# Kernel optimization log

Hardware: AMD Instinct MI355X
Metric: run time of the kernel (lower is better)

## Reference

```python
import jax, jax.numpy as jnp
import numpy as np

D_MODEL = 1024
N_HEADS = 16
HEAD_DIM = D_MODEL // N_HEADS


def setup_inputs() -> dict:
    key = jax.random.key(0)
    ks = jax.random.split(key, 9)
    B, S = 2, 2048
    s = 1.0 / np.sqrt(D_MODEL)
    return {
        "x": jax.random.normal(ks[0], (B, S, D_MODEL), dtype=jnp.float32),
        "Wq": jax.random.normal(ks[1], (D_MODEL, D_MODEL), dtype=jnp.float32) * s,
        "bq": jnp.zeros((D_MODEL,), dtype=jnp.float32),
        "Wk": jax.random.normal(ks[2], (D_MODEL, D_MODEL), dtype=jnp.float32) * s,
        "bk": jnp.zeros((D_MODEL,), dtype=jnp.float32),
        "Wv": jax.random.normal(ks[3], (D_MODEL, D_MODEL), dtype=jnp.float32) * s,
        "bv": jnp.zeros((D_MODEL,), dtype=jnp.float32),
        "Wo": jax.random.normal(ks[4], (D_MODEL, D_MODEL), dtype=jnp.float32) * s,
        "bo": jnp.zeros((D_MODEL,), dtype=jnp.float32),
    }


def reference(x, Wq, bq, Wk, bk, Wv, bv, Wo, bo):
    B, S, D = x.shape
    H, Hd = N_HEADS, HEAD_DIM
    # projections; torch Linear: x @ W^T + b -> here W stored as [in, out]
    q = (x @ Wq + bq).reshape(B, S, H, Hd).transpose(0, 2, 1, 3)  # [B,H,S,Hd]
    k = (x @ Wk + bk).reshape(B, S, H, Hd).transpose(0, 2, 1, 3)
    v = (x @ Wv + bv).reshape(B, S, H, Hd).transpose(0, 2, 1, 3)
    scores = jnp.einsum("bhsd,bhtd->bhst", q, k) / jnp.sqrt(jnp.float32(Hd))
    causal = jnp.tril(jnp.ones((S, S), dtype=bool))  # True = keep
    scores = jnp.where(causal, scores, jnp.float32(-jnp.inf))
    attn = jax.nn.softmax(scores, axis=-1)
    out = jnp.einsum("bhst,bhtd->bhsd", attn, v)  # [B,H,S,Hd]
    out = out.transpose(0, 2, 1, 3).reshape(B, S, D)
    return out @ Wo + bo
```

## Files before the change

### kernel.cpp

```cpp
#include <hip/hip_runtime.h>
#include <hip/hip_bf16.h>
#include <cmath>

#define D_MODEL 1024
#define N_HEADS 16
#define HEAD_DIM 64
#define SEQ 2048
#define BATCH 2
#define MROWS (BATCH * SEQ)

typedef __bf16 bf16;
typedef __bf16 bf16x8 __attribute__((ext_vector_type(8)));
typedef __bf16 bf16x4 __attribute__((ext_vector_type(4)));
typedef float f32x4 __attribute__((ext_vector_type(4)));

#define SWZG(row, cbyte) ((row) * 64 + ((cbyte) ^ ((((row) >> 1) & 3) << 4)))

#define GLOAD16(g, l)                                                        \
    __builtin_amdgcn_global_load_lds(                                        \
        (const __attribute__((address_space(1))) void*)(g),                  \
        (__attribute__((address_space(3))) void*)(l), 16, 0, 0)

#define EXP2F(x) __builtin_amdgcn_exp2f(x)

static __device__ __forceinline__ unsigned short bfbits(float f) {
    bf16 b = (bf16)f;
    return *(unsigned short*)&b;
}

__global__ __launch_bounds__(256) void cvt_x(const float* __restrict__ x,
                                             bf16* __restrict__ xb) {
    int i = blockIdx.x * 256 + threadIdx.x;
    float4 v = ((const float4*)x)[i];
    bf16x4 o = { (bf16)v.x, (bf16)v.y, (bf16)v.z, (bf16)v.w };
    ((bf16x4*)xb)[i] = o;
}

__global__ void cvt_wt(const float* __restrict__ Wq, const float* __restrict__ Wk,
                       const float* __restrict__ Wv, const float* __restrict__ Wo,
                       bf16* __restrict__ wt) {
    __shared__ float tile[32][33];
    int z = blockIdx.z;
    const float* W = (z == 0) ? Wq : (z == 1) ? Wk : (z == 2) ? Wv : Wo;
    int n0 = blockIdx.x * 32, k0 = blockIdx.y * 32;
    int tx = threadIdx.x, ty = threadIdx.y;
    tile[ty][tx] = W[(size_t)(k0 + ty) * D_MODEL + n0 + tx];
    __syncthreads();
    wt[(size_t)z * D_MODEL * D_MODEL + (size_t)(n0 + ty) * D_MODEL + k0 + tx] =
        (bf16)tile[tx][ty];
}

template <int MODE>
__global__ __launch_bounds__(512) void gemm_k(const bf16* __restrict__ A,
                                              const bf16* __restrict__ Bt,
                                              const float* __restrict__ b0,
                                              const float* __restrict__ b1,
                                              const float* __restrict__ b2,
                                              void* __restrict__ outp) {
    constexpr int BM = 128, BK = 32, KDIM = D_MODEL;
    __shared__ alignas(16) char SMEM[49152];
    char* Asb = SMEM;
    char* Bsb = SMEM + 24576;
    const int tid = threadIdx.x;
    const int wid = tid >> 6, lane = tid & 63;
    const int m0 = blockIdx.y * BM, n0 = blockIdx.x * BM;
    const int wr = (wid >> 1) * 32, wc = (wid & 1) * 64;
    const int ml = lane & 15;
    f32x4 acc[2][4] = {};

#define GSTAGE(K0, BUF)                                                       \
    {                                                                         \
        const int row = tid >> 2;                                             \
        const int col = (tid & 3) ^ ((row >> 1) & 3);                         \
        GLOAD16(&A[(size_t)(m0 + row) * KDIM + (K0) + col * 8],               \
                Asb + (BUF) * 8192 + tid * 16);                               \
        GLOAD16(&Bt[(size_t)(n0 + row) * KDIM + (K0) + col * 8],              \
                Bsb + (BUF) * 8192 + tid * 16);                               \
    }

    GSTAGE(0, 0);
    GSTAGE(BK, 1);
    int cur = 0;
    for (int k0 = 0; k0 < KDIM; k0 += BK) {
        if (k0 + 2 * BK < KDIM) {
            int nb = cur + 2;
            if (nb >= 3) nb -= 3;
            GSTAGE(k0 + 2 * BK, nb);
            asm volatile("s_waitcnt vmcnt(4)" ::: "memory");
        } else if (k0 + BK < KDIM) {
            asm volatile("s_waitcnt vmcnt(2)" ::: "memory");
        } else {
            asm volatile("s_waitcnt vmcnt(0)" ::: "memory");
        }
        __builtin_amdgcn_s_barrier();

        char* Ab = Asb + cur * 8192;
        char* Bb = Bsb + cur * 8192;
        const int cb = (lane >> 4) * 16;
        bf16x8 a[2], b[4];
#pragma unroll
        for (int m = 0; m < 2; ++m) {
            int r = wr + m * 16 + ml;
            a[m] = *(bf16x8*)(Ab + SWZG(r, cb));
        }
#pragma unroll
        for (int n = 0; n < 4; ++n) {
            int r = wc + n * 16 + ml;
            b[n] = *(bf16x8*)(Bb + SWZG(r, cb));
        }
#pragma unroll
        for (int m = 0; m < 2; ++m)
#pragma unroll
            for (int n = 0; n < 4; ++n)
                acc[m][n] = __builtin_amdgcn_mfma_f32_16x16x32_bf16(a[m], b[n], acc[m][n], 0, 0, 0);

        __builtin_amdgcn_s_barrier();
        cur = (cur == 2) ? 0 : cur + 1;
    }
#undef GSTAGE

    const int z = n0 >> 10;
    const float* bias = (MODE == 1) ? b0 : ((z == 0) ? b0 : (z == 1) ? b1 : b2);

    if (MODE == 0 && z == 2) {
        bf16* T = (bf16*)SMEM;
#pragma unroll
        for (int m = 0; m < 2; ++m)
#pragma unroll
            for (int n = 0; n < 4; ++n)
#pragma unroll
                for (int r = 0; r < 4; ++r) {
                    int mll = wr + m * 16 + (lane >> 4) * 4 + r;
                    int nl = wc + n * 16 + ml;
                    float val = acc[m][n][r] + bias[(n0 & 1023) + nl];
                    *(bf16*)((char*)T + nl * 256 + ((2 * mll) ^ ((nl & 7) << 4))) = (bf16)val;
                }
        __builtin_amdgcn_s_barrier();
        const int b_ = m0 >> 11;
        const int s_base = m0 & 2047;
#pragma unroll
        for (int c = 0; c < 4; ++c) {
            int idx = c * 512 + tid;
            int nl = idx >> 4, j = idx & 15;
            bf16x8 v = *(bf16x8*)((char*)T + nl * 256 + ((16 * j) ^ ((nl & 7) << 4)));
            int colN = (n0 & 1023) + nl;
            int head = colN >> 6, hd = colN & 63;
            *(bf16x8*)&((bf16*)outp)[(size_t)2 * 4194304 +
                                     ((size_t)(b_ * N_HEADS + head) * HEAD_DIM + hd) * SEQ +
                                     s_base + 8 * j] = v;
        }
        return;
    }

#pragma unroll
    for (int m = 0; m < 2; ++m)
#pragma unroll
        for (int n = 0; n < 4; ++n)
#pragma unroll
            for (int r = 0; r < 4; ++r) {
                int grow = m0 + wr + m * 16 + (lane >> 4) * 4 + r;
                int gcol = n0 + wc + n * 16 + ml;
                if (MODE == 0) {
                    int colN = gcol & 1023;
                    float val = acc[m][n][r] + bias[colN];
                    if (z == 0) val *= 0.18033688011112042f;
                    int b_ = grow >> 11, s_ = grow & 2047;
                    int h = colN >> 6, hd = colN & 63;
                    ((bf16*)outp)[(size_t)z * 4194304 +
                                  ((size_t)(b_ * N_HEADS + h) * SEQ + s_) * HEAD_DIM + hd] =
                        (bf16)val;
                } else {
                    float val = acc[m][n][r] + bias[gcol];
                    ((float*)outp)[(size_t)grow * D_MODEL + gcol] = val;
                }
            }
}

__global__ __launch_bounds__(256) void attn_k(const bf16* __restrict__ Qg,
                                              const bf16* __restrict__ Kg,
                                              const bf16* __restrict__ VTg,
                                              bf16* __restrict__ AO) {
    __shared__ alignas(16) bf16 Ks[2][64 * 64];
    __shared__ alignas(16) bf16 Vs[2][64 * 64];
    __shared__ alignas(16) unsigned int Pk[4][16][32];
    const int tid = threadIdx.x, wid = tid >> 6, lane = tid & 63;
    const int m = lane & 15, h = lane >> 4;
    const int idx = blockIdx.x;
    const int bh = idx & 31;
    const int a = (idx >> 5) & 7;
    const int qd = idx >> 8;
    const int hb = (qd == 0) ? (31 - a) : (qd == 1) ? (23 - a) : (qd == 2) ? (8 + a) : a;
    const int q0 = hb * 64 + wid * 16;
    const size_t base = (size_t)bh * SEQ * HEAD_DIM;
    const bf16* VT = VTg + (size_t)bh * HEAD_DIM * SEQ;
    const int swz = (m & 7) << 2;
    const int nt = hb + 1;

    bf16x8 aq[2];
#pragma unroll
    for (int kc = 0; kc < 2; ++kc)
        aq[kc] = *(const bf16x8*)
            &Qg[base + (size_t)(q0 + m) * HEAD_DIM + kc * 32 + h * 8];

    f32x4 o[4] = {};
    float mrow = -__builtin_inff();
    float lrow = 0.f;

#define STAGE(T0, BUF)                                                            \
    {                                                                             \
        _Pragma("unroll") for (int c = 0; c < 2; ++c) {                           \
            int chunk = c * 256 + tid;                                            \
            int row = chunk >> 3, sl = chunk & 7;                                 \
            GLOAD16(&Kg[base + (size_t)((T0) + row) * HEAD_DIM +                  \
                        8 * (sl ^ (row & 7))],                                    \
                    (char*)&Ks[BUF][0] + chunk * 16);                             \
            GLOAD16(&VT[(size_t)row * SEQ + (T0) + 8 * (sl ^ (row & 7))],         \
                    (char*)&Vs[BUF][0] + chunk * 16);                             \
        }                                                                         \
    }

    STAGE(0, 0);
    int cur = 0;
    for (int it = 0; it < nt; ++it) {
        if (it + 1 < nt) {
            STAGE((it + 1) * 64, cur ^ 1);
            asm volatile("s_waitcnt vmcnt(4)" ::: "memory");
        } else {
            asm volatile("s_waitcnt vmcnt(0)" ::: "memory");
        }
        __builtin_amdgcn_s_barrier();

        {
            const int t0 = it * 64;
            char* Kb = (char*)&Ks[cur][0];
            char* Vb = (char*)&Vs[cur][0];
            bf16x8 kf[4][2], vf[4][2];
#pragma unroll
            for (int tf = 0; tf < 4; ++tf)
#pragma unroll
                for (int kc = 0; kc < 2; ++kc)
                    kf[tf][kc] = *(bf16x8*)(Kb + (16 * tf + m) * 128 +
                                            (((4 * kc + h) ^ (m & 7)) << 4));
#pragma unroll
            for (int nf = 0; nf < 4; ++nf)
#pragma unroll
                for (int kc = 0; kc < 2; ++kc)
                    vf[nf][kc] = *(bf16x8*)(Vb + (16 * nf + m) * 128 +
                                            (((4 * kc + h) ^ (m & 7)) << 4));

            f32x4 s[4];
            __builtin_amdgcn_s_setprio(1);
#pragma unroll
            for (int tf = 0; tf < 4; ++tf) {
                f32x4 z = {};
                z = __builtin_amdgcn_mfma_f32_16x16x32_bf16(kf[tf][0], aq[0], z, 0, 0, 0);
                z = __builtin_amdgcn_mfma_f32_16x16x32_bf16(kf[tf][1], aq[1], z, 0, 0, 0);
                s[tf] = z;
            }
            __builtin_amdgcn_s_setprio(0);

            if (it == nt - 1) {
#pragma unroll
                for (int tf = 0; tf < 4; ++tf)
#pragma unroll
                    for (int r = 0; r < 4; ++r) {
                        int gq = q0 + m;
                        int gt = t0 + tf * 16 + h * 4 + r;
                        if (gt > gq) s[tf][r] = -__builtin_inff();
                    }
            }

            float mt[4];
#pragma unroll
            for (int tf = 0; tf < 4; ++tf)
                mt[tf] = fmaxf(fmaxf(s[tf][0], s[tf][1]), fmaxf(s[tf][2], s[tf][3]));
            float mx = fmaxf(fmaxf(mt[0], mt[1]), fmaxf(mt[2], mt[3]));
            mx = fmaxf(mx, __shfl_xor(mx, 16));
            mx = fmaxf(mx, __shfl_xor(mx, 32));
            if (!__all(mx <= mrow + 11.541560327f)) {
                float mn = fmaxf(mrow, mx);
                float sf = EXP2F(mrow - mn);
                mrow = mn;
                lrow *= sf;
                float sfr[4];
#pragma unroll
                for (int r = 0; r < 4; ++r) sfr[r] = __shfl(sf, 20 * h + r);
#pragma unroll
                for (int nf = 0; nf < 4; ++nf)
#pragma unroll
                    for (int r = 0; r < 4; ++r) o[nf][r] *= sfr[r];
            }
            float rt[4];
#pragma unroll
            for (int tf = 0; tf < 4; ++tf) {
#pragma unroll
                for (int r = 0; r < 4; ++r) s[tf][r] = EXP2F(s[tf][r] - mrow);
                rt[tf] = (s[tf][0] + s[tf][1]) + (s[tf][2] + s[tf][3]);
            }
            float rs = (rt[0] + rt[1]) + (rt[2] + rt[3]);
            rs += __shfl_xor(rs, 16);
            rs += __shfl_xor(rs, 32);
            lrow += rs;

#pragma unroll
            for (int tf = 0; tf < 4; ++tf)
#pragma unroll
                for (int rp = 0; rp < 2; ++rp) {
                    unsigned int w = ((unsigned int)bfbits(s[tf][2 * rp + 1]) << 16) |
                                     bfbits(s[tf][2 * rp]);
                    Pk[wid][m][(8 * tf + 2 * h + rp) ^ swz] = w;
                }

            __builtin_amdgcn_s_setprio(1);
#pragma unroll
            for (int kc = 0; kc < 2; ++kc) {
                bf16x8 ap = *(bf16x8*)&Pk[wid][m][(16 * kc + 4 * h) ^ swz];
#pragma unroll
                for (int nf = 0; nf < 4; ++nf)
                    o[nf] = __builtin_amdgcn_mfma_f32_16x16x32_bf16(
                        ap, vf[nf][kc], o[nf], 0, 0, 0);
            }
            __builtin_amdgcn_s_setprio(0);
        }
        __builtin_amdgcn_s_barrier();
        cur ^= 1;
    }
#undef STAGE

    const int b_ = bh >> 4, hh = bh & 15;
    float lcr[4];
#pragma unroll
    for (int r = 0; r < 4; ++r) lcr[r] = __shfl(lrow, 20 * h + r);
#pragma unroll
    for (int nf = 0; nf < 4; ++nf)
#pragma unroll
        for (int r = 0; r < 4; ++r) {
            float val = o[nf][r] / lcr[r];
            int s_ = q0 + h * 4 + r;
            AO[((size_t)(b_ * SEQ + s_)) * D_MODEL + hh * HEAD_DIM + nf * 16 + m] =
                (bf16)val;
        }
}

extern "C" void kernel_launch(void* const* d_in, const int* in_sizes, int n_in,
                              void* d_out, int out_size, void* d_ws, size_t ws_size,
                              hipStream_t stream) {
    const float* x  = (const float*)d_in[0];
    const float* Wq = (const float*)d_in[1];
    const float* bq = (const float*)d_in[2];
    const float* Wk = (const float*)d_in[3];
    const float* bk = (const float*)d_in[4];
    const float* Wv = (const float*)d_in[5];
    const float* bv = (const float*)d_in[6];
    const float* Wo = (const float*)d_in[7];
    const float* bo = (const float*)d_in[8];

    char* ws = (char*)d_ws;
    const size_t MB = 1u << 20;
    bf16* wt = (bf16*)ws;
    bf16* xb = (bf16*)(ws + 8 * MB);
    bf16* Qb = (bf16*)(ws + 16 * MB);
    bf16* AO = (bf16*)(ws + 40 * MB);

    const size_t WSTRIDE = (size_t)D_MODEL * D_MODEL;

    cvt_x<<<dim3(MROWS * D_MODEL / 4 / 256), dim3(256), 0, stream>>>(x, xb);
    cvt_wt<<<dim3(32, 32, 4), dim3(32, 32), 0, stream>>>(Wq, Wk, Wv, Wo, wt);

    gemm_k<0><<<dim3(24, 32), dim3(512), 0, stream>>>(xb, wt, bq, bk, bv, Qb);

    bf16* Kb = Qb + 4194304;
    bf16* VTb = Qb + 2 * 4194304;
    attn_k<<<dim3(1024), dim3(256), 0, stream>>>(Qb, Kb, VTb, AO);

    gemm_k<1><<<dim3(8, 32), dim3(512), 0, stream>>>(AO, wt + 3 * WSTRIDE, bo, bo, bo, d_out);
}
```

Baseline: 108.2 us.

## Double K tile to 64 with two-stage LDS buffering in projection GEMM

The GEMM K-step grows from 32 to 64, halving the number of loop iterations and barriers. The pipeline changes from triple buffering to double buffering, with a new 8-way XOR swizzle over 128-byte rows. Each thread now issues four global-to-LDS loads per stage, and the wait counter is kept at 4 so only the current stage must land. LDS use rises to 64KB per block, which may reduce occupancy, and the prefetch distance shrinks to one stage.

```diff
diff --git a/kernel.cpp b/kernel.cpp
--- a/kernel.cpp
+++ b/kernel.cpp
@@ -13,8 +13,6 @@
 typedef __bf16 bf16x8 __attribute__((ext_vector_type(8)));
 typedef __bf16 bf16x4 __attribute__((ext_vector_type(4)));
 typedef float f32x4 __attribute__((ext_vector_type(4)));
-
-#define SWZG(row, cbyte) ((row) * 64 + ((cbyte) ^ ((((row) >> 1) & 3) << 4)))
 
 #define GLOAD16(g, l)                                                        \
     __builtin_amdgcn_global_load_lds(                                        \
@@ -57,65 +55,66 @@
                                               const float* __restrict__ b1,
                                               const float* __restrict__ b2,
                                               void* __restrict__ outp) {
-    constexpr int BM = 128, BK = 32, KDIM = D_MODEL;
-    __shared__ alignas(16) char SMEM[49152];
+    constexpr int BM = 128, BK = 64, KDIM = D_MODEL;
+    __shared__ alignas(16) char SMEM[65536];
     char* Asb = SMEM;
-    char* Bsb = SMEM + 24576;
+    char* Bsb = SMEM + 32768;
     const int tid = threadIdx.x;
     const int wid = tid >> 6, lane = tid & 63;
     const int m0 = blockIdx.y * BM, n0 = blockIdx.x * BM;
     const int wr = (wid >> 1) * 32, wc = (wid & 1) * 64;
-    const int ml = lane & 15;
+    const int ml = lane & 15, hh = lane >> 4;
     f32x4 acc[2][4] = {};
 
 #define GSTAGE(K0, BUF)                                                       \
     {                                                                         \
-        const int row = tid >> 2;                                             \
-        const int col = (tid & 3) ^ ((row >> 1) & 3);                         \
-        GLOAD16(&A[(size_t)(m0 + row) * KDIM + (K0) + col * 8],               \
-                Asb + (BUF) * 8192 + tid * 16);                               \
-        GLOAD16(&Bt[(size_t)(n0 + row) * KDIM + (K0) + col * 8],              \
-                Bsb + (BUF) * 8192 + tid * 16);                               \
+        _Pragma("unroll") for (int c = 0; c < 2; ++c) {                       \
+            const int chunk = c * 512 + tid;                                  \
+            const int row = chunk >> 3, sl = chunk & 7;                       \
+            const int col8 = sl ^ (row & 7);                                  \
+            GLOAD16(&A[(size_t)(m0 + row) * KDIM + (K0) + col8 * 8],          \
+                    Asb + (BUF) * 16384 + chunk * 16);                        \
+            GLOAD16(&Bt[(size_t)(n0 + row) * KDIM + (K0) + col8 * 8],         \
+                    Bsb + (BUF) * 16384 + chunk * 16);                        \
+        }                                                                     \
     }
 
     GSTAGE(0, 0);
-    GSTAGE(BK, 1);
     int cur = 0;
     for (int k0 = 0; k0 < KDIM; k0 += BK) {
-        if (k0 + 2 * BK < KDIM) {
-            int nb = cur + 2;
-            if (nb >= 3) nb -= 3;
-            GSTAGE(k0 + 2 * BK, nb);
+        if (k0 + BK < KDIM) {
+            GSTAGE(k0 + BK, cur ^ 1);
             asm volatile("s_waitcnt vmcnt(4)" ::: "memory");
-        } else if (k0 + BK < KDIM) {
-            asm volatile("s_waitcnt vmcnt(2)" ::: "memory");
         } else {
             asm volatile("s_waitcnt vmcnt(0)" ::: "memory");
         }
         __builtin_amdgcn_s_barrier();
 
-        char* Ab = Asb + cur * 8192;
-        char* Bb = Bsb + cur * 8192;
-        const int cb = (lane >> 4) * 16;
-        bf16x8 a[2], b[4];
-#pragma unroll
-        for (int m = 0; m < 2; ++m) {
-            int r = wr + m * 16 + ml;
-            a[m] = *(bf16x8*)(Ab + SWZG(r, cb));
-        }
-#pragma unroll
-        for (int n = 0; n < 4; ++n) {
-            int r = wc + n * 16 + ml;
-            b[n] = *(bf16x8*)(Bb + SWZG(r, cb));
-        }
-#pragma unroll
-        for (int m = 0; m < 2; ++m)
-#pragma unroll
-            for (int n = 0; n < 4; ++n)
-                acc[m][n] = __builtin_amdgcn_mfma_f32_16x16x32_bf16(a[m], b[n], acc[m][n], 0, 0, 0);
-
-        __builtin_amdgcn_s_barrier();
-        cur = (cur == 2) ? 0 : cur + 1;
+        char* Ab = Asb + cur * 16384;
+        char* Bb = Bsb + cur * 16384;
+#pragma unroll
+        for (int kc = 0; kc < 2; ++kc) {
+            bf16x8 a[2], b[4];
+#pragma unroll
+            for (int m = 0; m < 2; ++m) {
+                int r = wr + m * 16 + ml;
+                a[m] = *(bf16x8*)(Ab + r * 128 + ((((kc << 2) | hh) ^ (r & 7)) << 4));
+            }
+#pragma unroll
+            for (int n = 0; n < 4; ++n) {
+                int r = wc + n * 16 + ml;
+                b[n] = *(bf16x8*)(Bb + r * 128 + ((((kc << 2) | hh) ^ (r & 7)) << 4));
+            }
+#pragma unroll
+            for (int m = 0; m < 2; ++m)
+#pragma unroll
+                for (int n = 0; n < 4; ++n)
+                    acc[m][n] =
+                        __builtin_amdgcn_mfma_f32_16x16x32_bf16(a[m], b[n], acc[m][n], 0, 0, 0);
+        }
+
+        __builtin_amdgcn_s_barrier();
+        cur ^= 1;
     }
 #undef GSTAGE
 
```

Result: faster. 100.8 us (-6.9%).
